# Performance work log

Measured on AMD Instinct MI355X. Metric: run time of the kernel, lower is better.

## Reference

```python
import jax, jax.numpy as jnp
import numpy as np

N = 51200      # total nodes
G = 256        # graphs in batch
NPG = 200      # nodes per graph
E = 409600     # intra-graph edges
EPG = E // G
F_IN, HID, HEADS, NCLS = 768, 128, 4, 2


def setup_inputs() -> dict:
    key = jax.random.key(0)
    ks = jax.random.split(key, 20)
    x = jax.random.normal(ks[0], (N, F_IN), jnp.float32)
    # edges strictly inside each graph, no self-loops (PyG batching semantics)
    gid = jnp.arange(E, dtype=jnp.int32) // EPG
    sl = jax.random.randint(ks[1], (E,), 0, NPG, dtype=jnp.int32)
    off = jax.random.randint(ks[2], (E,), 1, NPG, dtype=jnp.int32)
    dl = (sl + off) % NPG
    edge_index = jnp.stack([gid * NPG + sl, gid * NPG + dl])
    batch = jnp.arange(N, dtype=jnp.int32) // NPG

    def glorot(k, shape, fan_in):
        return jax.random.normal(k, shape, jnp.float32) * np.float32(1.0 / np.sqrt(fan_in))

    return {
        'x': x, 'edge_index': edge_index, 'batch': batch,
        'W1': glorot(ks[3], (F_IN, HEADS * HID), F_IN),
        'a_src1': glorot(ks[4], (HEADS, HID), HID),
        'a_dst1': glorot(ks[5], (HEADS, HID), HID),
        'b1': jnp.zeros((HEADS * HID,), jnp.float32),
        'W2': glorot(ks[6], (HEADS * HID, HID), HEADS * HID),
        'a_src2': glorot(ks[7], (1, HID), HID),
        'a_dst2': glorot(ks[8], (1, HID), HID),
        'b2': jnp.zeros((HID,), jnp.float32),
        'Wc': glorot(ks[9], (HID, 2), HID),
        'bc': jnp.zeros((2,), jnp.float32),
        'Wf1': glorot(ks[10], (HID, HID), HID),
        'bf1': jnp.zeros((HID,), jnp.float32),
        'Wf2': glorot(ks[11], (HID, NCLS), HID),
        'bf2': jnp.zeros((NCLS,), jnp.float32),
    }


def _segment_softmax(logits, seg, num):
    m = jax.ops.segment_max(logits, seg, num_segments=num)
    e = jnp.exp(logits - m[seg])
    s = jax.ops.segment_sum(e, seg, num_segments=num)
    return e / (s[seg] + 1e-16)


def _gat(x, src, dst, W, a_s, a_d, b, n):
    # PyG GATConv, eval mode (attention dropout off), self-loops already in src/dst
    H, C = a_s.shape
    h = (x @ W).reshape(n, H, C)                       # [n,H,C]
    a_src = (h * a_s).sum(-1)                          # [n,H]
    a_dst = (h * a_d).sum(-1)
    logits = jax.nn.leaky_relu(a_src[src] + a_dst[dst], 0.2)  # [Etot,H]
    alpha = _segment_softmax(logits, dst, n)
    out = jax.ops.segment_sum(h[src] * alpha[:, :, None], dst, num_segments=n)
    return out.reshape(n, H * C) + b


def reference(x, edge_index, batch, W1, a_src1, a_dst1, b1, W2, a_src2, a_dst2, b2,
              Wc, bc, Wf1, bf1, Wf2, bf2):
    src0, dst0 = edge_index[0], edge_index[1]
    loop = jnp.arange(N, dtype=src0.dtype)
    src = jnp.concatenate([src0, loop])
    dst = jnp.concatenate([dst0, loop])

    h1 = jax.nn.relu(_gat(x, src, dst, W1, a_src1, a_dst1, b1, N))     # [N,512]
    h2 = jax.nn.relu(_gat(h1, src, dst, W2, a_src2, a_dst2, b2, N))    # [N,128]

    S = jax.nn.softmax(h2 @ Wc + bc, axis=1)                           # [N,2]

    # aggregate(): per-graph S^T A S via per-edge outer products (A from original edges)
    eg = batch[src0]
    outer = S[src0][:, :, None] * S[dst0][:, None, :]                  # [E,2,2]
    agg = jax.ops.segment_sum(outer, eg, num_segments=G)               # [G,2,2]
    rnorm = jnp.clip(jnp.abs(agg).sum(axis=2, keepdims=True), 1e-5, None)  # F.normalize p=1 dim=1
    nadj = agg / rnorm
    diag = jnp.diagonal(nadj, axis1=1, axis2=2)                        # [G,2]
    aggregate_loss = jnp.mean(jnp.mean((diag - 1.0) ** 2, axis=1))     # MSE vs ones, averaged over graphs

    # subgraph embedding: first row of S_g^T x_g per graph
    sub = jax.ops.segment_sum(S[:, 0:1] * h2, batch, num_segments=G)   # [G,128]

    out = jax.nn.relu(sub @ Wf1 + bf1)                                 # eval: dropout off
    out = out @ Wf2 + bf2                                              # [G,2]
    return out, aggregate_loss
```

## Files before the change

kernel.cpp:

```cpp
#include <hip/hip_runtime.h>
#include <hip/hip_bf16.h>
#include <cstdint>

#define N_NODES 51200
#define N_GRAPH 256
#define NPG     200
#define N_EDGE  409600
#define EPG     1600
#define F_IN    768
#define HID     128
#define HEADS   4
#define HC      512

typedef __attribute__((ext_vector_type(8))) short short8;
typedef __attribute__((ext_vector_type(4))) float floatx4;

constexpr size_t OFF_H1B    = 0;
constexpr size_t OFF_H2B    = OFF_H1B + (size_t)N_NODES * HC * 2;
constexpr size_t OFF_H2F    = OFF_H2B + (size_t)N_NODES * HID * 2;
constexpr size_t OFF_WT1    = OFF_H2F + (size_t)N_NODES * HID * 4;
constexpr size_t OFF_WT2    = OFF_WT1 + (size_t)HC * F_IN * 2;
constexpr size_t OFF_S      = OFF_WT2 + (size_t)HID * HC * 2;
constexpr size_t OFF_AGG    = OFF_S + (size_t)N_NODES * 2 * 4;
constexpr size_t OFF_SUB    = OFF_AGG + (size_t)N_GRAPH * 4 * 4;

__device__ __forceinline__ float leaky(float x) { return x >= 0.0f ? x : 0.2f * x; }

__device__ __forceinline__ unsigned short f2bf(float f) {
    unsigned int u = __float_as_uint(f);
    u += 0x7fffu + ((u >> 16) & 1u);
    return (unsigned short)(u >> 16);
}
__device__ __forceinline__ float bflo(int p) { return __uint_as_float((unsigned)p << 16); }
__device__ __forceinline__ float bfhi(int p) { return __uint_as_float((unsigned)p & 0xffff0000u); }

__device__ __forceinline__ unsigned int cvtpk(float lo, float hi) {
    unsigned int r;
    asm("v_cvt_pk_bf16_f32 %0, %1, %2" : "=v"(r) : "v"(lo), "v"(hi));
    return r;
}

__device__ __forceinline__ void gl_lds16(const void* g, void* l) {
    __builtin_amdgcn_global_load_lds(
        (__attribute__((address_space(1))) void*)(g),
        (__attribute__((address_space(3))) void*)(l),
        16, 0, 0);
}

__device__ __forceinline__ void store_cvt(short* dst, float4 a, float4 b, float4 c, float4 d) {
    uint4 q0, q1;
    q0.x = cvtpk(a.x, a.y); q0.y = cvtpk(a.z, a.w);
    q0.z = cvtpk(b.x, b.y); q0.w = cvtpk(b.z, b.w);
    q1.x = cvtpk(c.x, c.y); q1.y = cvtpk(c.z, c.w);
    q1.z = cvtpk(d.x, d.y); q1.w = cvtpk(d.z, d.w);
    *(uint4*)dst = q0;
    *(uint4*)(dst + 128) = q1;
}

__global__ __launch_bounds__(256)
void transpose_cvt_kernel(const float* __restrict__ W, short* __restrict__ Wt,
                          int K, int Nn)
{
    int idx = blockIdx.x * 256 + threadIdx.x;
    if (idx >= K * Nn) return;
    int k = idx / Nn, n = idx % Nn;
    Wt[(size_t)n * K + k] = (short)f2bf(W[idx]);
}

template <bool A_BF16>
__global__ __launch_bounds__(256)
void gemm_mfma_kernel(const void* __restrict__ Av, const short* __restrict__ Bt,
                      unsigned short* __restrict__ C, int M, int Nn, int K)
{
    __shared__ __align__(16) short Bblob[3][4096];
    __shared__ __align__(16) short Ablob[A_BF16 ? 3 : 2][4096];
    const int tid = threadIdx.x;
    const int w = tid >> 6, l = tid & 63;

    const int nwg = gridDim.x;
    int wg = blockIdx.x;
    wg = (wg & 7) * (nwg >> 3) + (wg >> 3);
    const int nbx = Nn >> 7;
    const int m0 = (wg / nbx) * 128;
    const int n0 = (wg % nbx) * 128;
    const int wr = w >> 1, wc = w & 1;
    const int wofs = w * 1024;

    floatx4 acc[4][4];
#pragma unroll
    for (int i = 0; i < 4; ++i)
#pragma unroll
        for (int j = 0; j < 4; ++j) acc[i][j] = (floatx4)0.0f;

    const short* bgp = Bt + (size_t)(n0 + (w * 2) * 16 + (l & 15)) * K + ((l >> 4) * 8);
    const int nt = K >> 5;

    auto compute = [&](int ai, int bi) {
        short8 af[4], bfr[4];
#pragma unroll
        for (int mi = 0; mi < 4; ++mi)
            af[mi] = *(const short8*)&Ablob[ai][(wr * 4 + mi) * 512 + l * 8];
#pragma unroll
        for (int ni = 0; ni < 4; ++ni)
            bfr[ni] = *(const short8*)&Bblob[bi][(wc * 4 + ni) * 512 + l * 8];
#pragma unroll
        for (int mi = 0; mi < 4; ++mi)
#pragma unroll
            for (int ni = 0; ni < 4; ++ni)
                acc[mi][ni] = __builtin_amdgcn_mfma_f32_16x16x32_bf16(
                    af[mi], bfr[ni], acc[mi][ni], 0, 0, 0);
    };

    if constexpr (A_BF16) {
        const short* agp = (const short*)Av
            + (size_t)(m0 + (w * 2) * 16 + (l & 15)) * K + ((l >> 4) * 8);
        gl_lds16(agp,               &Ablob[0][wofs]);
        gl_lds16(agp + 16 * K,      &Ablob[0][wofs + 512]);
        gl_lds16(bgp,               &Bblob[0][wofs]);
        gl_lds16(bgp + 16 * K,      &Bblob[0][wofs + 512]);
        gl_lds16(agp + 32,          &Ablob[1][wofs]);
        gl_lds16(agp + 16 * K + 32, &Ablob[1][wofs + 512]);
        gl_lds16(bgp + 32,          &Bblob[1][wofs]);
        gl_lds16(bgp + 16 * K + 32, &Bblob[1][wofs + 512]);
        asm volatile("s_waitcnt vmcnt(4)" ::: "memory");
        __builtin_amdgcn_s_barrier();

        int cur3 = 0;
        for (int t = 0; t < nt; ++t) {
            int nn3 = cur3 + 2; if (nn3 >= 3) nn3 -= 3;
            if (t + 2 < nt) {
                const int kk = (t + 2) << 5;
                gl_lds16(agp + kk,          &Ablob[nn3][wofs]);
                gl_lds16(agp + 16 * K + kk, &Ablob[nn3][wofs + 512]);
                gl_lds16(bgp + kk,          &Bblob[nn3][wofs]);
                gl_lds16(bgp + 16 * K + kk, &Bblob[nn3][wofs + 512]);
            }
            compute(cur3, cur3);
            if (t + 1 < nt) {
                if (t + 2 < nt) asm volatile("s_waitcnt vmcnt(4) lgkmcnt(0)" ::: "memory");
                else            asm volatile("s_waitcnt vmcnt(0) lgkmcnt(0)" ::: "memory");
                __builtin_amdgcn_s_barrier();
            }
            cur3 += 1; if (cur3 == 3) cur3 = 0;
        }
    } else {
        const float* Af = (const float*)Av;
        const int r = tid >> 1, hh = tid & 1;
        const float* arow = Af + (size_t)(m0 + r) * K + hh * 16;
        const int oA = (r >> 4) * 512 + (2 * hh) * 128 + (r & 15) * 8;

        float4 sa0, sa1, sa2, sa3, sb0, sb1, sb2, sb3, sc0, sc1, sc2, sc3;

#define LOADA4(P0, P1, P2, P3, T) { const float* ap_ = arow + ((T) << 5); \
        P0 = *(const float4*)(ap_ + 0); P1 = *(const float4*)(ap_ + 4);   \
        P2 = *(const float4*)(ap_ + 8); P3 = *(const float4*)(ap_ + 12); }

        gl_lds16(bgp,               &Bblob[0][wofs]);
        gl_lds16(bgp + 16 * K,      &Bblob[0][wofs + 512]);
        gl_lds16(bgp + 32,          &Bblob[1][wofs]);
        gl_lds16(bgp + 16 * K + 32, &Bblob[1][wofs + 512]);
        LOADA4(sa0, sa1, sa2, sa3, 0);
        LOADA4(sb0, sb1, sb2, sb3, 1);
        LOADA4(sc0, sc1, sc2, sc3, 2);
        asm volatile("s_waitcnt vmcnt(8)" ::: "memory");
        store_cvt(&Ablob[0][oA], sa0, sa1, sa2, sa3);
        asm volatile("s_waitcnt lgkmcnt(0)" ::: "memory");
        __builtin_amdgcn_s_barrier();

        int cur3 = 0;
#define GITER(T, SS0, SS1, SS2, SS3, SL0, SL1, SL2, SL3) {                      \
        const int t_ = (T);                                                     \
        if (t_ < nt) {                                                          \
            int nn3 = cur3 + 2; if (nn3 >= 3) nn3 -= 3;                         \
            if (t_ + 2 < nt) {                                                  \
                const int kk = (t_ + 2) << 5;                                   \
                gl_lds16(bgp + kk,          &Bblob[nn3][wofs]);                 \
                gl_lds16(bgp + 16 * K + kk, &Bblob[nn3][wofs + 512]);           \
            }                                                                   \
            if (t_ + 3 < nt) LOADA4(SL0, SL1, SL2, SL3, t_ + 3);                \
            compute(t_ & 1, cur3);                                              \
            if (t_ + 1 < nt) {                                                  \
                store_cvt(&Ablob[(t_ + 1) & 1][oA], SS0, SS1, SS2, SS3);        \
                if (t_ + 3 < nt)                                                \
                    asm volatile("s_waitcnt vmcnt(10) lgkmcnt(0)" ::: "memory");\
                else if (t_ + 2 < nt)                                           \
                    asm volatile("s_waitcnt vmcnt(6) lgkmcnt(0)" ::: "memory"); \
                else                                                            \
                    asm volatile("s_waitcnt vmcnt(0) lgkmcnt(0)" ::: "memory"); \
                __builtin_amdgcn_s_barrier();                                   \
            }                                                                   \
            cur3 += 1; if (cur3 == 3) cur3 = 0;                                 \
        } }

        for (int t3 = 0; t3 < nt; t3 += 3) {
            GITER(t3 + 0, sb0, sb1, sb2, sb3, sa0, sa1, sa2, sa3);
            GITER(t3 + 1, sc0, sc1, sc2, sc3, sb0, sb1, sb2, sb3);
            GITER(t3 + 2, sa0, sa1, sa2, sa3, sc0, sc1, sc2, sc3);
        }
#undef GITER
#undef LOADA4
    }

    const int lr = (l >> 4) * 4, lc = l & 15;
#pragma unroll
    for (int mi = 0; mi < 4; ++mi)
#pragma unroll
        for (int ni = 0; ni < 4; ++ni) {
            const size_t base = (size_t)(m0 + wr * 64 + mi * 16 + lr) * Nn
                              + (n0 + wc * 64 + ni * 16 + lc);
#pragma unroll
            for (int rr = 0; rr < 4; ++rr)
                C[base + (size_t)rr * Nn] = f2bf(acc[mi][ni][rr]);
        }
}

__global__ __launch_bounds__(512)
void gat1_kernel(const unsigned short* __restrict__ H, const int* __restrict__ src0,
                 const int* __restrict__ dst0, const float* __restrict__ a_s,
                 const float* __restrict__ a_d, const float* __restrict__ b1,
                 unsigned short* __restrict__ out)
{
    const int g = blockIdx.x, h = blockIdx.y;
    __shared__ int   s_feat[NPG * 64];
    __shared__ float s_as[NPG], s_ad[NPG], s_m[NPG], s_inv[NPG];
    __shared__ int   s_row[NPG + 1];
    __shared__ int   s_cnt[NPG];
    __shared__ int   s_scan[256];
    __shared__ unsigned short s_eraw[EPG];
    __shared__ int2  s_wc[EPG];
    const int tid = threadIdx.x, w = tid >> 6, l = tid & 63;
    const int gbase = g * NPG;

    for (int flat = tid; flat < NPG * 16; flat += 512) {
        int row = flat >> 4, q = flat & 15;
        uint4 v = *(const uint4*)(H + (size_t)(gbase + row) * HC + h * HID + q * 8);
        *(uint4*)&s_feat[row * 64 + q * 4] = v;
    }
    for (int j = tid; j < EPG; j += 512) {
        int s = src0[g * EPG + j] - gbase;
        int d = dst0[g * EPG + j] - gbase;
        s_eraw[j] = (unsigned short)(s | (d << 8));
    }
    if (tid < NPG) s_cnt[tid] = 0;
    __syncthreads();

    for (int j = tid; j < EPG; j += 512)
        atomicAdd(&s_cnt[s_eraw[j] >> 8], 1);
    const float2 av = ((const float2*)(a_s + h * HID))[l];
    const float2 dv = ((const float2*)(a_d + h * HID))[l];
    for (int nl = w; nl < NPG; nl += 8) {
        int pk = s_feat[nl * 64 + l];
        float f0 = bflo(pk), f1 = bfhi(pk);
        float ss = f0 * av.x + f1 * av.y;
        float sd = f0 * dv.x + f1 * dv.y;
#pragma unroll
        for (int off = 1; off < 64; off <<= 1) {
            ss += __shfl_xor(ss, off);
            sd += __shfl_xor(sd, off);
        }
        if (l == 0) { s_as[nl] = ss; s_ad[nl] = sd; }
    }
    __syncthreads();

    {
        int v = (tid < NPG) ? s_cnt[tid] : 0;
        if (tid < 256) s_scan[tid] = v;
        __syncthreads();
        for (int off = 1; off < 256; off <<= 1) {
            int u = (tid >= off && tid < 256) ? s_scan[tid - off] : 0;
            __syncthreads();
            if (tid < 256) s_scan[tid] += u;
            __syncthreads();
        }
        if (tid < NPG) s_row[tid + 1] = s_scan[tid];
        if (tid == 0) s_row[0] = 0;
        __syncthreads();
        if (tid < NPG) s_scan[tid] = s_row[tid];
    }
    __syncthreads();

    for (int j = tid; j < EPG; j += 512) {
        int pk = s_eraw[j];
        int p = atomicAdd(&s_scan[pk >> 8], 1);
        s_wc[p].y = pk;
    }
    __syncthreads();

    for (int j = tid; j < EPG; j += 512) {
        int pk = s_wc[j].y;
        s_wc[j].x = __float_as_int(leaky(s_as[pk & 255] + s_ad[pk >> 8]));
    }
    __syncthreads();

    if (tid < NPG) {
        float m = leaky(s_as[tid] + s_ad[tid]);
        int r0 = s_row[tid], r1 = s_row[tid + 1];
        for (int j = r0; j < r1; ++j) m = fmaxf(m, __int_as_float(s_wc[j].x));
        s_m[tid] = m;
    }
    __syncthreads();

    for (int j = tid; j < EPG; j += 512) {
        int2 e = s_wc[j];
        s_wc[j].x = __float_as_int(__expf(__int_as_float(e.x) - s_m[e.y >> 8]));
    }
    __syncthreads();

    if (tid < NPG) {
        float rs = __expf(leaky(s_as[tid] + s_ad[tid]) - s_m[tid]);
        int r0 = s_row[tid], r1 = s_row[tid + 1];
        for (int j = r0; j < r1; ++j) rs += __int_as_float(s_wc[j].x);
        s_inv[tid] = 1.0f / (rs + 1e-16f);
    }
    __syncthreads();

    const float2 bv = ((const float2*)(b1 + h * HID))[l];
    for (int nl = w; nl < NPG; nl += 8) {
        const int r0 = s_row[nl], r1 = s_row[nl + 1];
        const float wself = __expf(leaky(s_as[nl] + s_ad[nl]) - s_m[nl]);
        int spk = s_feat[nl * 64 + l];
        float a0 = wself * bflo(spk), a1 = wself * bfhi(spk);
        float c0 = 0.0f, c1 = 0.0f;
        int j = r0;
        for (; j + 4 <= r1; j += 4) {
            int2 e0 = s_wc[j], e1 = s_wc[j + 1], e2 = s_wc[j + 2], e3 = s_wc[j + 3];
            int p0 = s_feat[(e0.y & 255) * 64 + l];
            int p1 = s_feat[(e1.y & 255) * 64 + l];
            int p2 = s_feat[(e2.y & 255) * 64 + l];
            int p3 = s_feat[(e3.y & 255) * 64 + l];
            float w0 = __int_as_float(e0.x), w1 = __int_as_float(e1.x);
            float w2 = __int_as_float(e2.x), w3 = __int_as_float(e3.x);
            a0 += w0 * bflo(p0); a1 += w0 * bfhi(p0);
            c0 += w1 * bflo(p1); c1 += w1 * bfhi(p1);
            a0 += w2 * bflo(p2); a1 += w2 * bfhi(p2);
            c0 += w3 * bflo(p3); c1 += w3 * bfhi(p3);
        }
        for (; j < r1; ++j) {
            int2 e0 = s_wc[j];
            int p0 = s_feat[(e0.y & 255) * 64 + l];
            float w0 = __int_as_float(e0.x);
            a0 += w0 * bflo(p0); a1 += w0 * bfhi(p0);
        }
        const float inv = s_inv[nl];
        float o0 = (a0 + c0) * inv + bv.x;
        float o1 = (a1 + c1) * inv + bv.y;
        unsigned int st = (unsigned int)f2bf(fmaxf(o0, 0.0f))
                        | ((unsigned int)f2bf(fmaxf(o1, 0.0f)) << 16);
        *(unsigned int*)&out[(size_t)(gbase + nl) * HC + h * HID + 2 * l] = st;
    }
}

__global__ __launch_bounds__(512)
void gat2_kernel(const unsigned short* __restrict__ H, const int* __restrict__ src0,
                 const int* __restrict__ dst0, const float* __restrict__ a_s,
                 const float* __restrict__ a_d, const float* __restrict__ b2,
                 const float* __restrict__ Wc, const float* __restrict__ bc,
                 float* __restrict__ h2, float* __restrict__ S)
{
    const int g = blockIdx.x;
    __shared__ int   s_feat[NPG * 64];
    __shared__ float s_as[NPG], s_ad[NPG], s_m[NPG], s_inv[NPG];
    __shared__ int   s_row[NPG + 1];
    __shared__ int   s_cnt[NPG];
    __shared__ int   s_scan[256];
    __shared__ unsigned short s_eraw[EPG];
    __shared__ int2  s_wc[EPG];
    const int tid = threadIdx.x, w = tid >> 6, l = tid & 63;
    const int gbase = g * NPG;

    for (int flat = tid; flat < NPG * 16; flat += 512) {
        int row = flat >> 4, q = flat & 15;
        uint4 v = *(const uint4*)(H + (size_t)(gbase + row) * HID + q * 8);
        *(uint4*)&s_feat[row * 64 + q * 4] = v;
    }
    for (int j = tid; j < EPG; j += 512) {
        int s = src0[g * EPG + j] - gbase;
        int d = dst0[g * EPG + j] - gbase;
        s_eraw[j] = (unsigned short)(s | (d << 8));
    }
    if (tid < NPG) s_cnt[tid] = 0;
    __syncthreads();

    for (int j = tid; j < EPG; j += 512)
        atomicAdd(&s_cnt[s_eraw[j] >> 8], 1);
    const float2 av = ((const float2*)a_s)[l];
    const float2 dv = ((const float2*)a_d)[l];
    for (int nl = w; nl < NPG; nl += 8) {
        int pk = s_feat[nl * 64 + l];
        float f0 = bflo(pk), f1 = bfhi(pk);
        float ss = f0 * av.x + f1 * av.y;
        float sd = f0 * dv.x + f1 * dv.y;
#pragma unroll
        for (int off = 1; off < 64; off <<= 1) {
            ss += __shfl_xor(ss, off);
            sd += __shfl_xor(sd, off);
        }
        if (l == 0) { s_as[nl] = ss; s_ad[nl] = sd; }
    }
    __syncthreads();

    {
        int v = (tid < NPG) ? s_cnt[tid] : 0;
        if (tid < 256) s_scan[tid] = v;
        __syncthreads();
        for (int off = 1; off < 256; off <<= 1) {
            int u = (tid >= off && tid < 256) ? s_scan[tid - off] : 0;
            __syncthreads();
            if (tid < 256) s_scan[tid] += u;
            __syncthreads();
        }
        if (tid < NPG) s_row[tid + 1] = s_scan[tid];
        if (tid == 0) s_row[0] = 0;
        __syncthreads();
        if (tid < NPG) s_scan[tid] = s_row[tid];
    }
    __syncthreads();

    for (int j = tid; j < EPG; j += 512) {
        int pk = s_eraw[j];
        int p = atomicAdd(&s_scan[pk >> 8], 1);
        s_wc[p].y = pk;
    }
    __syncthreads();

    for (int j = tid; j < EPG; j += 512) {
        int pk = s_wc[j].y;
        s_wc[j].x = __float_as_int(leaky(s_as[pk & 255] + s_ad[pk >> 8]));
    }
    __syncthreads();

    if (tid < NPG) {
        float m = leaky(s_as[tid] + s_ad[tid]);
        int r0 = s_row[tid], r1 = s_row[tid + 1];
        for (int j = r0; j < r1; ++j) m = fmaxf(m, __int_as_float(s_wc[j].x));
        s_m[tid] = m;
    }
    __syncthreads();

    for (int j = tid; j < EPG; j += 512) {
        int2 e = s_wc[j];
        s_wc[j].x = __float_as_int(__expf(__int_as_float(e.x) - s_m[e.y >> 8]));
    }
    __syncthreads();

    if (tid < NPG) {
        float rs = __expf(leaky(s_as[tid] + s_ad[tid]) - s_m[tid]);
        int r0 = s_row[tid], r1 = s_row[tid + 1];
        for (int j = r0; j < r1; ++j) rs += __int_as_float(s_wc[j].x);
        s_inv[tid] = 1.0f / (rs + 1e-16f);
    }
    __syncthreads();

    const float2 bv = ((const float2*)b2)[l];
    const float4 wcv = ((const float4*)Wc)[l];
    const float bc0 = bc[0], bc1 = bc[1];
    for (int nl = w; nl < NPG; nl += 8) {
        const int r0 = s_row[nl], r1 = s_row[nl + 1];
        const float wself = __expf(leaky(s_as[nl] + s_ad[nl]) - s_m[nl]);
        int spk = s_feat[nl * 64 + l];
        float a0 = wself * bflo(spk), a1 = wself * bfhi(spk);
        float c0 = 0.0f, c1 = 0.0f;
        int j = r0;
        for (; j + 4 <= r1; j += 4) {
            int2 e0 = s_wc[j], e1 = s_wc[j + 1], e2 = s_wc[j + 2], e3 = s_wc[j + 3];
            int p0 = s_feat[(e0.y & 255) * 64 + l];
            int p1 = s_feat[(e1.y & 255) * 64 + l];
            int p2 = s_feat[(e2.y & 255) * 64 + l];
            int p3 = s_feat[(e3.y & 255) * 64 + l];
            float w0 = __int_as_float(e0.x), w1 = __int_as_float(e1.x);
            float w2 = __int_as_float(e2.x), w3 = __int_as_float(e3.x);
            a0 += w0 * bflo(p0); a1 += w0 * bfhi(p0);
            c0 += w1 * bflo(p1); c1 += w1 * bfhi(p1);
            a0 += w2 * bflo(p2); a1 += w2 * bfhi(p2);
            c0 += w3 * bflo(p3); c1 += w3 * bfhi(p3);
        }
        for (; j < r1; ++j) {
            int2 e0 = s_wc[j];
            int p0 = s_feat[(e0.y & 255) * 64 + l];
            float w0 = __int_as_float(e0.x);
            a0 += w0 * bflo(p0); a1 += w0 * bfhi(p0);
        }
        const float inv = s_inv[nl];
        float o0 = fmaxf((a0 + c0) * inv + bv.x, 0.0f);
        float o1 = fmaxf((a1 + c1) * inv + bv.y, 0.0f);
        *(float2*)&h2[(size_t)(gbase + nl) * HID + 2 * l] = make_float2(o0, o1);
        float z0 = o0 * wcv.x + o1 * wcv.z;
        float z1 = o0 * wcv.y + o1 * wcv.w;
#pragma unroll
        for (int off = 1; off < 64; off <<= 1) {
            z0 += __shfl_xor(z0, off);
            z1 += __shfl_xor(z1, off);
        }
        if (l == 0) {
            z0 += bc0; z1 += bc1;
            float mm = fmaxf(z0, z1);
            float e0 = __expf(z0 - mm), e1 = __expf(z1 - mm);
            float is = 1.0f / (e0 + e1);
            *(float2*)&S[(size_t)(gbase + nl) * 2] = make_float2(e0 * is, e1 * is);
        }
    }
}

__global__ __launch_bounds__(256)
void agg_kernel(const int* __restrict__ src0, const int* __restrict__ dst0,
                const float* __restrict__ S, float* __restrict__ agg)
{
    const int g = blockIdx.x, tid = threadIdx.x;
    float a00 = 0, a01 = 0, a10 = 0, a11 = 0;
    for (int e = g*EPG + tid; e < (g + 1)*EPG; e += 256) {
        int s = src0[e], d = dst0[e];
        float s0 = S[s*2], s1 = S[s*2 + 1];
        float d0 = S[d*2], d1 = S[d*2 + 1];
        a00 += s0*d0; a01 += s0*d1; a10 += s1*d0; a11 += s1*d1;
    }
    for (int off = 32; off > 0; off >>= 1) {
        a00 += __shfl_down(a00, off); a01 += __shfl_down(a01, off);
        a10 += __shfl_down(a10, off); a11 += __shfl_down(a11, off);
    }
    __shared__ float sred[4][4];
    if ((tid & 63) == 0) {
        int w = tid >> 6;
        sred[w][0] = a00; sred[w][1] = a01; sred[w][2] = a10; sred[w][3] = a11;
    }
    __syncthreads();
    if (tid == 0) {
        agg[g*4 + 0] = sred[0][0] + sred[1][0] + sred[2][0] + sred[3][0];
        agg[g*4 + 1] = sred[0][1] + sred[1][1] + sred[2][1] + sred[3][1];
        agg[g*4 + 2] = sred[0][2] + sred[1][2] + sred[2][2] + sred[3][2];
        agg[g*4 + 3] = sred[0][3] + sred[1][3] + sred[2][3] + sred[3][3];
    }
}

__global__ __launch_bounds__(256)
void loss_kernel(const float* __restrict__ agg, float* __restrict__ out_loss)
{
    int tid = threadIdx.x;
    float a00 = agg[tid*4 + 0], a01 = agg[tid*4 + 1];
    float a10 = agg[tid*4 + 2], a11 = agg[tid*4 + 3];
    float rn0 = fmaxf(fabsf(a00) + fabsf(a01), 1e-5f);
    float rn1 = fmaxf(fabsf(a10) + fabsf(a11), 1e-5f);
    float d0 = a00 / rn0 - 1.0f, d1 = a11 / rn1 - 1.0f;
    float contrib = 0.5f * (d0*d0 + d1*d1);
    for (int off = 32; off > 0; off >>= 1) contrib += __shfl_down(contrib, off);
    __shared__ float sred[4];
    if ((tid & 63) == 0) sred[tid >> 6] = contrib;
    __syncthreads();
    if (tid == 0)
        out_loss[0] = (sred[0] + sred[1] + sred[2] + sred[3]) * (1.0f / N_GRAPH);
}

__global__ __launch_bounds__(128)
void sub_kernel(const float* __restrict__ S, const float* __restrict__ h2,
                float* __restrict__ sub)
{
    const int g = blockIdx.x, c = threadIdx.x;
    const float* Sg = S + (size_t)g * NPG * 2;
    const float* hg = h2 + (size_t)g * NPG * HID;
    float acc = 0.0f;
    for (int i = 0; i < NPG; ++i)
        acc += Sg[i*2] * hg[(size_t)i*HID + c];
    sub[g*HID + c] = acc;
}

__global__ __launch_bounds__(128)
void final_kernel(const float* __restrict__ sub, const float* __restrict__ Wf1,
                  const float* __restrict__ bf1, const float* __restrict__ Wf2,
                  const float* __restrict__ bf2, float* __restrict__ out)
{
    __shared__ float s_sub[128];
    __shared__ float s_fc[128];
    const int g = blockIdx.x, t = threadIdx.x;
    s_sub[t] = sub[g*HID + t];
    __syncthreads();
    float acc = bf1[t];
    for (int c = 0; c < 128; ++c)
        acc += s_sub[c] * Wf1[c*128 + t];
    s_fc[t] = fmaxf(acc, 0.0f);
    __syncthreads();
    if (t < 2) {
        float z = bf2[t];
        for (int j = 0; j < 128; ++j) z += s_fc[j] * Wf2[j*2 + t];
        out[g*2 + t] = z;
    }
}

extern "C" void kernel_launch(void* const* d_in, const int* in_sizes, int n_in,
                              void* d_out, int out_size, void* d_ws, size_t ws_size,
                              hipStream_t stream)
{
    const float* x   = (const float*)d_in[0];
    const int*   ei  = (const int*)d_in[1];
    const float* W1  = (const float*)d_in[3];
    const float* as1 = (const float*)d_in[4];
    const float* ad1 = (const float*)d_in[5];
    const float* b1  = (const float*)d_in[6];
    const float* W2  = (const float*)d_in[7];
    const float* as2 = (const float*)d_in[8];
    const float* ad2 = (const float*)d_in[9];
    const float* b2  = (const float*)d_in[10];
    const float* Wc  = (const float*)d_in[11];
    const float* bc  = (const float*)d_in[12];
    const float* Wf1 = (const float*)d_in[13];
    const float* bf1 = (const float*)d_in[14];
    const float* Wf2 = (const float*)d_in[15];
    const float* bf2 = (const float*)d_in[16];
    const int* src0 = ei;
    const int* dst0 = ei + N_EDGE;

    char* ws = (char*)d_ws;
    unsigned short* H1b = (unsigned short*)(ws + OFF_H1B);
    unsigned short* H2b = (unsigned short*)(ws + OFF_H2B);
    float* h2    = (float*)(ws + OFF_H2F);
    short* Wt1   = (short*)(ws + OFF_WT1);
    short* Wt2   = (short*)(ws + OFF_WT2);
    float* Sbuf  = (float*)(ws + OFF_S);
    float* aggb  = (float*)(ws + OFF_AGG);
    float* subb  = (float*)(ws + OFF_SUB);
    float* out   = (float*)d_out;

    transpose_cvt_kernel<<<(F_IN*HC + 255)/256, 256, 0, stream>>>(W1, Wt1, F_IN, HC);
    transpose_cvt_kernel<<<(HC*HID + 255)/256, 256, 0, stream>>>(W2, Wt2, HC, HID);

    gemm_mfma_kernel<false><<<(N_NODES/128) * (HC/128), 256, 0, stream>>>(
        x, Wt1, H1b, N_NODES, HC, F_IN);

    gat1_kernel<<<dim3(N_GRAPH, HEADS), 512, 0, stream>>>(
        H1b, src0, dst0, as1, ad1, b1, H1b);

    gemm_mfma_kernel<true><<<(N_NODES/128) * (HID/128), 256, 0, stream>>>(
        H1b, Wt2, H2b, N_NODES, HID, HC);

    gat2_kernel<<<N_GRAPH, 512, 0, stream>>>(
        H2b, src0, dst0, as2, ad2, b2, Wc, bc, h2, Sbuf);

    agg_kernel<<<N_GRAPH, 256, 0, stream>>>(src0, dst0, Sbuf, aggb);
    loss_kernel<<<1, 256, 0, stream>>>(aggb, out + N_GRAPH*2);

    sub_kernel<<<N_GRAPH, 128, 0, stream>>>(Sbuf, h2, subb);
    final_kernel<<<N_GRAPH, 128, 0, stream>>>(subb, Wf1, bf1, Wf2, bf2, out);

    (void)in_sizes; (void)n_in; (void)out_size; (void)ws_size;
}
```

Measured before the change: 501.8 us.

## Fuse aggregate and subgraph reductions into GAT2; stage fp32 A via async LDS loads

The agg and sub kernels are folded into the second GAT kernel. It now computes S per node, accumulates the S0-weighted sum of h2 and the per-edge S outer products from shared memory, and never writes h2 or S to global memory. The first GEMM now loads the fp32 x tile straight into LDS with global_load_lds and converts it to bf16 when reading fragments, instead of staging through registers. That GEMM uses a double-buffered pipeline, and both GEMMs get launch bounds of 3 blocks per CU. The trade-off is more LDS per GEMM block and extra shared memory plus reductions in gat2, in exchange for two fewer launches and much less global traffic.

```diff
diff --git a/kernel.cpp b/kernel.cpp
--- a/kernel.cpp
+++ b/kernel.cpp
@@ -47,16 +47,6 @@
         16, 0, 0);
 }
 
-__device__ __forceinline__ void store_cvt(short* dst, float4 a, float4 b, float4 c, float4 d) {
-    uint4 q0, q1;
-    q0.x = cvtpk(a.x, a.y); q0.y = cvtpk(a.z, a.w);
-    q0.z = cvtpk(b.x, b.y); q0.w = cvtpk(b.z, b.w);
-    q1.x = cvtpk(c.x, c.y); q1.y = cvtpk(c.z, c.w);
-    q1.z = cvtpk(d.x, d.y); q1.w = cvtpk(d.z, d.w);
-    *(uint4*)dst = q0;
-    *(uint4*)(dst + 128) = q1;
-}
-
 __global__ __launch_bounds__(256)
 void transpose_cvt_kernel(const float* __restrict__ W, short* __restrict__ Wt,
                           int K, int Nn)
@@ -67,13 +57,105 @@
     Wt[(size_t)n * K + k] = (short)f2bf(W[idx]);
 }
 
-template <bool A_BF16>
-__global__ __launch_bounds__(256)
-void gemm_mfma_kernel(const void* __restrict__ Av, const short* __restrict__ Bt,
+__global__ __launch_bounds__(256, 3)
+void gemm_xw1_kernel(const float* __restrict__ A, const short* __restrict__ Bt,
+                     unsigned short* __restrict__ C, int M, int Nn, int K)
+{
+    __shared__ __align__(16) float Asm[2][128 * 32];
+    __shared__ __align__(16) short Bsm[2][4096];
+    const int tid = threadIdx.x;
+    const int w = tid >> 6, l = tid & 63;
+
+    const int nwg = gridDim.x;
+    int wg = blockIdx.x;
+    wg = (wg & 7) * (nwg >> 3) + (wg >> 3);
+    const int nbx = Nn >> 7;
+    const int m0 = (wg / nbx) * 128;
+    const int n0 = (wg % nbx) * 128;
+    const int wr = w >> 1, wc = w & 1;
+
+    floatx4 acc[4][4];
+#pragma unroll
+    for (int i = 0; i < 4; ++i)
+#pragma unroll
+        for (int j = 0; j < 4; ++j) acc[i][j] = (floatx4)0.0f;
+
+    const short* bgp = Bt + (size_t)(n0 + w * 32 + (l & 15)) * K + ((l >> 4) * 8);
+    const float* agp = A + (size_t)(m0 + w * 32 + (l & 7)) * K + ((l >> 3) * 4);
+    const int nt = K >> 5;
+
+    int aB[4];
+#pragma unroll
+    for (int mi = 0; mi < 4; ++mi)
+        aB[mi] = (wr * 8 + mi * 2 + ((l & 15) >> 3)) * 256 + (l >> 4) * 64 + (l & 7) * 4;
+    const int bB0 = wc * 2048 + l * 8;
+
+#define STAGE1(buf, t) {                                                        \
+        const int ko_ = (t) * 32;                                               \
+        gl_lds16(agp + ko_,              &Asm[buf][w * 1024]);                  \
+        gl_lds16(agp + 8 * K + ko_,      &Asm[buf][w * 1024 + 256]);            \
+        gl_lds16(agp + 16 * K + ko_,     &Asm[buf][w * 1024 + 512]);            \
+        gl_lds16(agp + 24 * K + ko_,     &Asm[buf][w * 1024 + 768]);            \
+        gl_lds16(bgp + ko_,              &Bsm[buf][w * 1024]);                  \
+        gl_lds16(bgp + 16 * K + ko_,     &Bsm[buf][w * 1024 + 512]); }
+
+#define COMPUTE1(buf) {                                                         \
+        short8 af[4], bfr[4];                                                   \
+        _Pragma("unroll")                                                       \
+        for (int mi = 0; mi < 4; ++mi) {                                        \
+            float4 v0 = *(const float4*)&Asm[buf][aB[mi]];                      \
+            float4 v1 = *(const float4*)&Asm[buf][aB[mi] + 32];                 \
+            uint4 pk;                                                           \
+            pk.x = cvtpk(v0.x, v0.y); pk.y = cvtpk(v0.z, v0.w);                 \
+            pk.z = cvtpk(v1.x, v1.y); pk.w = cvtpk(v1.z, v1.w);                 \
+            af[mi] = *reinterpret_cast<short8*>(&pk);                           \
+        }                                                                       \
+        _Pragma("unroll")                                                       \
+        for (int ni = 0; ni < 4; ++ni)                                          \
+            bfr[ni] = *(const short8*)&Bsm[buf][bB0 + ni * 512];                \
+        _Pragma("unroll")                                                       \
+        for (int mi = 0; mi < 4; ++mi)                                          \
+            _Pragma("unroll")                                                   \
+            for (int ni = 0; ni < 4; ++ni)                                      \
+                acc[mi][ni] = __builtin_amdgcn_mfma_f32_16x16x32_bf16(          \
+                    af[mi], bfr[ni], acc[mi][ni], 0, 0, 0); }
+
+    STAGE1(0, 0);
+    asm volatile("s_waitcnt vmcnt(0)" ::: "memory");
+    __builtin_amdgcn_s_barrier();
+
+    int cur = 0;
+    for (int t = 0; t < nt; ++t) {
+        if (t + 1 < nt) STAGE1(cur ^ 1, t + 1);
+        COMPUTE1(cur);
+        if (t + 1 < nt) {
+            asm volatile("s_waitcnt vmcnt(0) lgkmcnt(0)" ::: "memory");
+            __builtin_amdgcn_s_barrier();
+            cur ^= 1;
+        }
+    }
+#undef STAGE1
+#undef COMPUTE1
+
+    const int lr = (l >> 4) * 4, lc = l & 15;
+#pragma unroll
+    for (int mi = 0; mi < 4; ++mi)
+#pragma unroll
+        for (int ni = 0; ni < 4; ++ni) {
+            const size_t base = (size_t)(m0 + wr * 64 + mi * 16 + lr) * Nn
+                              + (n0 + wc * 64 + ni * 16 + lc);
+#pragma unroll
+            for (int rr = 0; rr < 4; ++rr)
+                C[base + (size_t)rr * Nn] = f2bf(acc[mi][ni][rr]);
+        }
+}
+
+__global__ __launch_bounds__(256, 3)
+void gemm_bf16_kernel(const short* __restrict__ Ab, const short* __restrict__ Bt,
                       unsigned short* __restrict__ C, int M, int Nn, int K)
 {
     __shared__ __align__(16) short Bblob[3][4096];
-    __shared__ __align__(16) short Ablob[A_BF16 ? 3 : 2][4096];
+    __shared__ __align__(16) short Ablob[3][4096];
     const int tid = threadIdx.x;
     const int w = tid >> 6, l = tid & 63;
 
@@ -92,14 +174,15 @@
 #pragma unroll
         for (int j = 0; j < 4; ++j) acc[i][j] = (floatx4)0.0f;
 
-    const short* bgp = Bt + (size_t)(n0 + (w * 2) * 16 + (l & 15)) * K + ((l >> 4) * 8);
+    const short* bgp = Bt + (size_t)(n0 + w * 32 + (l & 15)) * K + ((l >> 4) * 8);
+    const short* agp = Ab + (size_t)(m0 + w * 32 + (l & 15)) * K + ((l >> 4) * 8);
     const int nt = K >> 5;
 
-    auto compute = [&](int ai, int bi) {
+    auto compute = [&](int bi) {
         short8 af[4], bfr[4];
 #pragma unroll
         for (int mi = 0; mi < 4; ++mi)
-            af[mi] = *(const short8*)&Ablob[ai][(wr * 4 + mi) * 512 + l * 8];
+            af[mi] = *(const short8*)&Ablob[bi][(wr * 4 + mi) * 512 + l * 8];
 #pragma unroll
         for (int ni = 0; ni < 4; ++ni)
             bfr[ni] = *(const short8*)&Bblob[bi][(wc * 4 + ni) * 512 + l * 8];
@@ -111,94 +194,34 @@
                     af[mi], bfr[ni], acc[mi][ni], 0, 0, 0);
     };
 
-    if constexpr (A_BF16) {
-        const short* agp = (const short*)Av
-            + (size_t)(m0 + (w * 2) * 16 + (l & 15)) * K + ((l >> 4) * 8);
-        gl_lds16(agp,               &Ablob[0][wofs]);
-        gl_lds16(agp + 16 * K,      &Ablob[0][wofs + 512]);
-        gl_lds16(bgp,               &Bblob[0][wofs]);
-        gl_lds16(bgp + 16 * K,      &Bblob[0][wofs + 512]);
-        gl_lds16(agp + 32,          &Ablob[1][wofs]);
-        gl_lds16(agp + 16 * K + 32, &Ablob[1][wofs + 512]);
-        gl_lds16(bgp + 32,          &Bblob[1][wofs]);
-        gl_lds16(bgp + 16 * K + 32, &Bblob[1][wofs + 512]);
-        asm volatile("s_waitcnt vmcnt(4)" ::: "memory");
-        __builtin_amdgcn_s_barrier();
-
-        int cur3 = 0;
-        for (int t = 0; t < nt; ++t) {
-            int nn3 = cur3 + 2; if (nn3 >= 3) nn3 -= 3;
-            if (t + 2 < nt) {
-                const int kk = (t + 2) << 5;
-                gl_lds16(agp + kk,          &Ablob[nn3][wofs]);
-                gl_lds16(agp + 16 * K + kk, &Ablob[nn3][wofs + 512]);
-                gl_lds16(bgp + kk,          &Bblob[nn3][wofs]);
-                gl_lds16(bgp + 16 * K + kk, &Bblob[nn3][wofs + 512]);
-            }
-            compute(cur3, cur3);
-            if (t + 1 < nt) {
-                if (t + 2 < nt) asm volatile("s_waitcnt vmcnt(4) lgkmcnt(0)" ::: "memory");
-                else            asm volatile("s_waitcnt vmcnt(0) lgkmcnt(0)" ::: "memory");
-                __builtin_amdgcn_s_barrier();
-            }
-            cur3 += 1; if (cur3 == 3) cur3 = 0;
-        }
-    } else {
-        const float* Af = (const float*)Av;
-        const int r = tid >> 1, hh = tid & 1;
-        const float* arow = Af + (size_t)(m0 + r) * K + hh * 16;
-        const int oA = (r >> 4) * 512 + (2 * hh) * 128 + (r & 15) * 8;
-
-        float4 sa0, sa1, sa2, sa3, sb0, sb1, sb2, sb3, sc0, sc1, sc2, sc3;
-
-#define LOADA4(P0, P1, P2, P3, T) { const float* ap_ = arow + ((T) << 5); \
-        P0 = *(const float4*)(ap_ + 0); P1 = *(const float4*)(ap_ + 4);   \
-        P2 = *(const float4*)(ap_ + 8); P3 = *(const float4*)(ap_ + 12); }
-
-        gl_lds16(bgp,               &Bblob[0][wofs]);
-        gl_lds16(bgp + 16 * K,      &Bblob[0][wofs + 512]);
-        gl_lds16(bgp + 32,          &Bblob[1][wofs]);
-        gl_lds16(bgp + 16 * K + 32, &Bblob[1][wofs + 512]);
-        LOADA4(sa0, sa1, sa2, sa3, 0);
-        LOADA4(sb0, sb1, sb2, sb3, 1);
-        LOADA4(sc0, sc1, sc2, sc3, 2);
-        asm volatile("s_waitcnt vmcnt(8)" ::: "memory");
-        store_cvt(&Ablob[0][oA], sa0, sa1, sa2, sa3);
-        asm volatile("s_waitcnt lgkmcnt(0)" ::: "memory");
-        __builtin_amdgcn_s_barrier();
-
-        int cur3 = 0;
-#define GITER(T, SS0, SS1, SS2, SS3, SL0, SL1, SL2, SL3) {                      \
-        const int t_ = (T);                                                     \
-        if (t_ < nt) {                                                          \
-            int nn3 = cur3 + 2; if (nn3 >= 3) nn3 -= 3;                         \
-            if (t_ + 2 < nt) {                                                  \
-                const int kk = (t_ + 2) << 5;                                   \
-                gl_lds16(bgp + kk,          &Bblob[nn3][wofs]);                 \
-                gl_lds16(bgp + 16 * K + kk, &Bblob[nn3][wofs + 512]);           \
-            }                                                                   \
-            if (t_ + 3 < nt) LOADA4(SL0, SL1, SL2, SL3, t_ + 3);                \
-            compute(t_ & 1, cur3);                                              \
-            if (t_ + 1 < nt) {                                                  \
-                store_cvt(&Ablob[(t_ + 1) & 1][oA], SS0, SS1, SS2, SS3);        \
-                if (t_ + 3 < nt)                                                \
-                    asm volatile("s_waitcnt vmcnt(10) lgkmcnt(0)" ::: "memory");\
-                else if (t_ + 2 < nt)                                           \
-                    asm volatile("s_waitcnt vmcnt(6) lgkmcnt(0)" ::: "memory"); \
-                else                                                            \
-                    asm volatile("s_waitcnt vmcnt(0) lgkmcnt(0)" ::: "memory"); \
-                __builtin_amdgcn_s_barrier();                                   \
-            }                                                                   \
-            cur3 += 1; if (cur3 == 3) cur3 = 0;                                 \
-        } }
-
-        for (int t3 = 0; t3 < nt; t3 += 3) {
-            GITER(t3 + 0, sb0, sb1, sb2, sb3, sa0, sa1, sa2, sa3);
-            GITER(t3 + 1, sc0, sc1, sc2, sc3, sb0, sb1, sb2, sb3);
-            GITER(t3 + 2, sa0, sa1, sa2, sa3, sc0, sc1, sc2, sc3);
-        }
-#undef GITER
-#undef LOADA4
+    gl_lds16(agp,               &Ablob[0][wofs]);
+    gl_lds16(agp + 16 * K,      &Ablob[0][wofs + 512]);
+    gl_lds16(bgp,               &Bblob[0][wofs]);
+    gl_lds16(bgp + 16 * K,      &Bblob[0][wofs + 512]);
+    gl_lds16(agp + 32,          &Ablob[1][wofs]);
+    gl_lds16(agp + 16 * K + 32, &Ablob[1][wofs + 512]);
+    gl_lds16(bgp + 32,          &Bblob[1][wofs]);
+    gl_lds16(bgp + 16 * K + 32, &Bblob[1][wofs + 512]);
+    asm volatile("s_waitcnt vmcnt(4)" ::: "memory");
+    __builtin_amdgcn_s_barrier();
+
+    int cur3 = 0;
+    for (int t = 0; t < nt; ++t) {
+        int nn3 = cur3 + 2; if (nn3 >= 3) nn3 -= 3;
+        if (t + 2 < nt) {
+            const int kk = (t + 2) << 5;
+            gl_lds16(agp + kk,          &Ablob[nn3][wofs]);
+            gl_lds16(agp + 16 * K + kk, &Ablob[nn3][wofs + 512]);
+            gl_lds16(bgp + kk,          &Bblob[nn3][wofs]);
+            gl_lds16(bgp + 16 * K + kk, &Bblob[nn3][wofs + 512]);
+        }
+        compute(cur3);
+        if (t + 1 < nt) {
+            if (t + 2 < nt) asm volatile("s_waitcnt vmcnt(4) lgkmcnt(0)" ::: "memory");
+            else            asm volatile("s_waitcnt vmcnt(0) lgkmcnt(0)" ::: "memory");
+            __builtin_amdgcn_s_barrier();
+        }
+        cur3 += 1; if (cur3 == 3) cur3 = 0;
     }
 
     const int lr = (l >> 4) * 4, lc = l & 15;
@@ -355,7 +378,7 @@
                  const int* __restrict__ dst0, const float* __restrict__ a_s,
                  const float* __restrict__ a_d, const float* __restrict__ b2,
                  const float* __restrict__ Wc, const float* __restrict__ bc,
-                 float* __restrict__ h2, float* __restrict__ S)
+                 float* __restrict__ sub, float* __restrict__ agg)
 {
     const int g = blockIdx.x;
     __shared__ int   s_feat[NPG * 64];
@@ -365,6 +388,9 @@
     __shared__ int   s_scan[256];
     __shared__ unsigned short s_eraw[EPG];
     __shared__ int2  s_wc[EPG];
+    __shared__ float2 s_Sv[NPG];
+    __shared__ float  s_red[8 * 128];
+    __shared__ float  s_aggr[8][4];
     const int tid = threadIdx.x, w = tid >> 6, l = tid & 63;
     const int gbase = g * NPG;
 
@@ -454,6 +480,7 @@
     const float2 bv = ((const float2*)b2)[l];
     const float4 wcv = ((const float4*)Wc)[l];
     const float bc0 = bc[0], bc1 = bc[1];
+    float accs0 = 0.0f, accs1 = 0.0f;
     for (int nl = w; nl < NPG; nl += 8) {
         const int r0 = s_row[nl], r1 = s_row[nl + 1];
         const float wself = __expf(leaky(s_as[nl] + s_ad[nl]) - s_m[nl]);
@@ -483,7 +510,6 @@
         const float inv = s_inv[nl];
         float o0 = fmaxf((a0 + c0) * inv + bv.x, 0.0f);
         float o1 = fmaxf((a1 + c1) * inv + bv.y, 0.0f);
-        *(float2*)&h2[(size_t)(gbase + nl) * HID + 2 * l] = make_float2(o0, o1);
         float z0 = o0 * wcv.x + o1 * wcv.z;
         float z1 = o0 * wcv.y + o1 * wcv.w;
 #pragma unroll
@@ -491,43 +517,46 @@
             z0 += __shfl_xor(z0, off);
             z1 += __shfl_xor(z1, off);
         }
-        if (l == 0) {
-            z0 += bc0; z1 += bc1;
-            float mm = fmaxf(z0, z1);
-            float e0 = __expf(z0 - mm), e1 = __expf(z1 - mm);
-            float is = 1.0f / (e0 + e1);
-            *(float2*)&S[(size_t)(gbase + nl) * 2] = make_float2(e0 * is, e1 * is);
-        }
-    }
-}
-
-__global__ __launch_bounds__(256)
-void agg_kernel(const int* __restrict__ src0, const int* __restrict__ dst0,
-                const float* __restrict__ S, float* __restrict__ agg)
-{
-    const int g = blockIdx.x, tid = threadIdx.x;
+        z0 += bc0; z1 += bc1;
+        float mm = fmaxf(z0, z1);
+        float e0 = __expf(z0 - mm), e1 = __expf(z1 - mm);
+        float is = 1.0f / (e0 + e1);
+        float s0v = e0 * is, s1v = e1 * is;
+        if (l == 0) s_Sv[nl] = make_float2(s0v, s1v);
+        accs0 += s0v * o0;
+        accs1 += s0v * o1;
+    }
+    s_red[w * 128 + 2 * l]     = accs0;
+    s_red[w * 128 + 2 * l + 1] = accs1;
+    __syncthreads();
+
     float a00 = 0, a01 = 0, a10 = 0, a11 = 0;
-    for (int e = g*EPG + tid; e < (g + 1)*EPG; e += 256) {
-        int s = src0[e], d = dst0[e];
-        float s0 = S[s*2], s1 = S[s*2 + 1];
-        float d0 = S[d*2], d1 = S[d*2 + 1];
-        a00 += s0*d0; a01 += s0*d1; a10 += s1*d0; a11 += s1*d1;
-    }
+    for (int j = tid; j < EPG; j += 512) {
+        int pk = s_eraw[j];
+        float2 Ss = s_Sv[pk & 255];
+        float2 Sd = s_Sv[pk >> 8];
+        a00 += Ss.x * Sd.x; a01 += Ss.x * Sd.y;
+        a10 += Ss.y * Sd.x; a11 += Ss.y * Sd.y;
+    }
+#pragma unroll
     for (int off = 32; off > 0; off >>= 1) {
         a00 += __shfl_down(a00, off); a01 += __shfl_down(a01, off);
         a10 += __shfl_down(a10, off); a11 += __shfl_down(a11, off);
     }
-    __shared__ float sred[4][4];
-    if ((tid & 63) == 0) {
-        int w = tid >> 6;
-        sred[w][0] = a00; sred[w][1] = a01; sred[w][2] = a10; sred[w][3] = a11;
-    }
-    __syncthreads();
-    if (tid == 0) {
-        agg[g*4 + 0] = sred[0][0] + sred[1][0] + sred[2][0] + sred[3][0];
-        agg[g*4 + 1] = sred[0][1] + sred[1][1] + sred[2][1] + sred[3][1];
-        agg[g*4 + 2] = sred[0][2] + sred[1][2] + sred[2][2] + sred[3][2];
-        agg[g*4 + 3] = sred[0][3] + sred[1][3] + sred[2][3] + sred[3][3];
+    if (l == 0) { s_aggr[w][0] = a00; s_aggr[w][1] = a01; s_aggr[w][2] = a10; s_aggr[w][3] = a11; }
+    __syncthreads();
+
+    if (tid < 128) {
+        float s = 0.0f;
+#pragma unroll
+        for (int w8 = 0; w8 < 8; ++w8) s += s_red[w8 * 128 + tid];
+        sub[(size_t)g * HID + tid] = s;
+    }
+    if (tid < 4) {
+        float s = 0.0f;
+#pragma unroll
+        for (int w8 = 0; w8 < 8; ++w8) s += s_aggr[w8][tid];
+        agg[g * 4 + tid] = s;
     }
 }
 
@@ -547,19 +576,6 @@
     __syncthreads();
     if (tid == 0)
         out_loss[0] = (sred[0] + sred[1] + sred[2] + sred[3]) * (1.0f / N_GRAPH);
-}
-
-__global__ __launch_bounds__(128)
-void sub_kernel(const float* __restrict__ S, const float* __restrict__ h2,
-                float* __restrict__ sub)
-{
-    const int g = blockIdx.x, c = threadIdx.x;
-    const float* Sg = S + (size_t)g * NPG * 2;
-    const float* hg = h2 + (size_t)g * NPG * HID;
-    float acc = 0.0f;
-    for (int i = 0; i < NPG; ++i)
-        acc += Sg[i*2] * hg[(size_t)i*HID + c];
-    sub[g*HID + c] = acc;
 }
 
 __global__ __launch_bounds__(128)
@@ -610,10 +626,8 @@
     char* ws = (char*)d_ws;
     unsigned short* H1b = (unsigned short*)(ws + OFF_H1B);
     unsigned short* H2b = (unsigned short*)(ws + OFF_H2B);
-    float* h2    = (float*)(ws + OFF_H2F);
     short* Wt1   = (short*)(ws + OFF_WT1);
     short* Wt2   = (short*)(ws + OFF_WT2);
-    float* Sbuf  = (float*)(ws + OFF_S);
     float* aggb  = (float*)(ws + OFF_AGG);
     float* subb  = (float*)(ws + OFF_SUB);
     float* out   = (float*)d_out;
@@ -621,22 +635,19 @@
     transpose_cvt_kernel<<<(F_IN*HC + 255)/256, 256, 0, stream>>>(W1, Wt1, F_IN, HC);
     transpose_cvt_kernel<<<(HC*HID + 255)/256, 256, 0, stream>>>(W2, Wt2, HC, HID);
 
-    gemm_mfma_kernel<false><<<(N_NODES/128) * (HC/128), 256, 0, stream>>>(
+    gemm_xw1_kernel<<<(N_NODES/128) * (HC/128), 256, 0, stream>>>(
         x, Wt1, H1b, N_NODES, HC, F_IN);
 
     gat1_kernel<<<dim3(N_GRAPH, HEADS), 512, 0, stream>>>(
         H1b, src0, dst0, as1, ad1, b1, H1b);
 
-    gemm_mfma_kernel<true><<<(N_NODES/128) * (HID/128), 256, 0, stream>>>(
-        H1b, Wt2, H2b, N_NODES, HID, HC);
+    gemm_bf16_kernel<<<(N_NODES/128) * (HID/128), 256, 0, stream>>>(
+        (const short*)H1b, Wt2, H2b, N_NODES, HID, HC);
 
     gat2_kernel<<<N_GRAPH, 512, 0, stream>>>(
-        H2b, src0, dst0, as2, ad2, b2, Wc, bc, h2, Sbuf);
-
-    agg_kernel<<<N_GRAPH, 256, 0, stream>>>(src0, dst0, Sbuf, aggb);
+        H2b, src0, dst0, as2, ad2, b2, Wc, bc, subb, aggb);
+
     loss_kernel<<<1, 256, 0, stream>>>(aggb, out + N_GRAPH*2);
-
-    sub_kernel<<<N_GRAPH, 128, 0, stream>>>(Sbuf, h2, subb);
     final_kernel<<<N_GRAPH, 128, 0, stream>>>(subb, Wf1, bf1, Wf2, bf2, out);
 
     (void)in_sizes; (void)n_in; (void)out_size; (void)ws_size;
```

After: 510.4 us. No clear change (+1.7%).
